# Optimization experiments

Hardware: AMD Instinct MI355X
Metric: run time of the kernel (lower is better)

## Reference

```python
import jax, jax.numpy as jnp
import numpy as np

B, N, DEG = 128, 512, 16          # graphs, nodes/graph, avg degree
NB = B * N                        # 65536 nodes
E = NB * DEG                      # 1048576 edges
K1, K2, K3 = 410, 205, 103        # ceil(0.8*512), ceil(0.5*410), ceil(0.5*205)
H, C = 4, 32                      # GAT heads, head dim
F_IN, ED = 128, 7


def _glorot(key, shape, fan_in):
    return jax.random.normal(key, shape, dtype=jnp.float32) / np.float32(np.sqrt(fan_in))


def setup_inputs() -> dict:
    key = jax.random.key(0)
    ks = jax.random.split(key, 24)
    x = jax.random.normal(ks[0], (NB, F_IN), dtype=jnp.float32)
    # random intra-graph edges, then offset per graph
    src = jax.random.randint(ks[1], (E,), 0, N)
    dst = jax.random.randint(ks[2], (E,), 0, N)
    off = jnp.repeat(jnp.arange(B) * N, N * DEG)
    edge_index = jnp.stack([src + off, dst + off]).astype(jnp.int32)
    edge_attr = jax.random.normal(ks[3], (E, ED), dtype=jnp.float32)
    p = {
        'c1_wl': _glorot(ks[4], (F_IN, F_IN), F_IN), 'c1_bl': jnp.zeros((F_IN,), jnp.float32), 'c1_wr': _glorot(ks[5], (F_IN, F_IN), F_IN),
        'p1_w': _glorot(ks[6], (F_IN,), F_IN),
        'c2_wl': _glorot(ks[7], (F_IN, F_IN), F_IN), 'c2_bl': jnp.zeros((F_IN,), jnp.float32), 'c2_wr': _glorot(ks[8], (F_IN, F_IN), F_IN),
        'p2_wrel': _glorot(ks[9], (F_IN, 1), F_IN), 'p2_brel': jnp.zeros((1,), jnp.float32), 'p2_wroot': _glorot(ks[10], (F_IN, 1), F_IN),
        'g_w': _glorot(ks[11], (F_IN, H * C), F_IN), 'g_as': _glorot(ks[12], (H, C), C), 'g_ad': _glorot(ks[13], (H, C), C),
        'g_we': _glorot(ks[14], (ED, H * C), ED), 'g_ae': _glorot(ks[15], (H, C), C), 'g_b': jnp.zeros((H * C,), jnp.float32),
        'p3_wrel': _glorot(ks[16], (F_IN, 1), F_IN), 'p3_brel': jnp.zeros((1,), jnp.float32), 'p3_wroot': _glorot(ks[17], (F_IN, 1), F_IN),
        'l1_w': _glorot(ks[18], (F_IN, F_IN), F_IN), 'l1_b': jnp.zeros((F_IN,), jnp.float32),
        'l2_w': _glorot(ks[19], (F_IN, 64), F_IN), 'l2_b': jnp.zeros((64,), jnp.float32),
        'l3_w': _glorot(ks[20], (64, 1), 64), 'l3_b': jnp.zeros((1,), jnp.float32),
    }
    return {'x': x, 'edge_index': edge_index, 'edge_attr': edge_attr, **p}


def _sage(x, src, dst, emf, wl, bl, wr):
    # SAGEConv: mean-aggregate neighbors (masked edges), lin_l(agg)+lin_r(x)
    agg = jax.ops.segment_sum(x[src] * emf[:, None], dst, num_segments=NB)
    cnt = jax.ops.segment_sum(emf, dst, num_segments=NB)
    mean = agg / jnp.maximum(cnt, 1.0)[:, None]
    return mean @ wl + bl + x @ wr


def _graphconv(x, src, dst, emf, wrel, brel, wroot):
    # GraphConv (SAGPooling score GNN): add-aggregation
    agg = jax.ops.segment_sum(x[src] * emf[:, None], dst, num_segments=NB)
    return (agg @ wrel + brel + x @ wroot).reshape(-1)


def _pool(x, score, nmask, K):
    # per-graph static top-k (equal-size graphs) == PyG topk + filter
    masked = jnp.where(nmask, score, -jnp.inf).reshape(B, N)
    idx = jax.lax.top_k(masked, K)[1]
    nm = jnp.zeros((B, N), dtype=bool).at[jnp.arange(B)[:, None], idx].set(True).reshape(-1)
    x = jnp.where(nm[:, None], x * score[:, None], 0.0)
    return x, nm


def _gap(x, K):
    # global mean pool; dropped nodes are exactly zero, K live nodes per graph
    return x.reshape(B, N, F_IN).sum(axis=1) / K


def _gat(x, src, dst, emf, nmask, edge_attr, w, a_s, a_d, w_e, a_e, b):
    xs = (x @ w).reshape(NB, H, C)
    al_s = (xs * a_s).sum(-1)                                   # [NB,H]
    al_d = (xs * a_d).sum(-1)
    al_e = ((edge_attr @ w_e).reshape(E, H, C) * a_e).sum(-1)    # [E,H]
    alpha = jax.nn.leaky_relu(al_s[src] + al_d[dst] + al_e, 0.2)
    alpha = jnp.where(emf[:, None] > 0, alpha, -jnp.inf)
    # PyG add_self_loops=True with fill_value='mean' for edge_attr
    ea_mean = (edge_attr * emf[:, None]).sum(0) / jnp.maximum(emf.sum(), 1.0)
    al_se = ((ea_mean @ w_e).reshape(H, C) * a_e).sum(-1)        # [H]
    alpha_self = jax.nn.leaky_relu(al_s + al_d + al_se[None, :], 0.2)
    alpha_self = jnp.where(nmask[:, None], alpha_self, -jnp.inf)
    m = jnp.maximum(jax.ops.segment_max(alpha, dst, num_segments=NB), alpha_self)
    m = jnp.where(jnp.isfinite(m), m, 0.0)
    ex = jnp.exp(alpha - m[dst]) * emf[:, None]
    ex_s = jnp.where(nmask[:, None], jnp.exp(alpha_self - m), 0.0)
    den = jnp.maximum(jax.ops.segment_sum(ex, dst, num_segments=NB) + ex_s, 1e-16)
    num = jax.ops.segment_sum(ex[:, :, None] * xs[src], dst, num_segments=NB) + ex_s[:, :, None] * xs
    return (num / den[:, :, None]).reshape(NB, H * C) + b


def _forward(x, edge_index, edge_attr, c1_wl, c1_bl, c1_wr, p1_w, c2_wl, c2_bl, c2_wr,
             p2_wrel, p2_brel, p2_wroot, g_w, g_as, g_ad, g_we, g_ae, g_b,
             p3_wrel, p3_brel, p3_wroot, l1_w, l1_b, l2_w, l2_b, l3_w, l3_b):
    src, dst = edge_index[0], edge_index[1]
    nmask = jnp.ones((NB,), dtype=bool)
    emf = jnp.ones((E,), jnp.float32)

    # block 1: SAGEConv -> TopKPooling(0.8) -> gap
    x = jax.nn.relu(_sage(x, src, dst, emf, c1_wl, c1_bl, c1_wr))
    s1 = jnp.tanh((x @ p1_w) / jnp.linalg.norm(p1_w))
    x, nmask = _pool(x, s1, nmask, K1)
    emf = emf * nmask[src] * nmask[dst]
    x1 = _gap(x, K1)

    # block 2: SAGEConv -> SAGPooling(0.5) -> gap
    x = jax.nn.relu(_sage(x, src, dst, emf, c2_wl, c2_bl, c2_wr))
    s2 = jnp.tanh(_graphconv(x, src, dst, emf, p2_wrel, p2_brel, p2_wroot))
    x, nmask = _pool(x, s2, nmask, K2)
    emf = emf * nmask[src] * nmask[dst]
    x2 = _gap(x, K2)

    # block 3: GATConv(128->32x4, edge_dim=7) -> SAGPooling(0.5) -> gap
    x = jax.nn.relu(_gat(x, src, dst, emf, nmask, edge_attr, g_w, g_as, g_ad, g_we, g_ae, g_b))
    s3 = jnp.tanh(_graphconv(x, src, dst, emf, p3_wrel, p3_brel, p3_wroot))
    x, nmask = _pool(x, s3, nmask, K3)
    x3 = _gap(x, K3)

    h = x1 + x2 + x3
    h = jax.nn.relu(h @ l1_w + l1_b)
    h = jax.nn.relu(h @ l2_w + l2_b)   # dropout identity in eval
    return jax.nn.sigmoid(h @ l3_w + l3_b)[:, 0]


def reference(x, edge_index, edge_attr, c1_wl, c1_bl, c1_wr, p1_w, c2_wl, c2_bl, c2_wr,
              p2_wrel, p2_brel, p2_wroot, g_w, g_as, g_ad, g_we, g_ae, g_b,
              p3_wrel, p3_brel, p3_wroot, l1_w, l1_b, l2_w, l2_b, l3_w, l3_b):
    return _forward(x, edge_index, edge_attr, c1_wl, c1_bl, c1_wr, p1_w, c2_wl, c2_bl, c2_wr,
                    p2_wrel, p2_brel, p2_wroot, g_w, g_as, g_ad, g_we, g_ae, g_b,
                    p3_wrel, p3_brel, p3_wroot, l1_w, l1_b, l2_w, l2_b, l3_w, l3_b)
```

## Files before the change

kernel.cpp:

```cpp
#include <hip/hip_runtime.h>
#include <math.h>

#define NBV 65536
#define EV  1048576
#define BV  128
#define K1V 410
#define K2V 205
#define K3V 103
#define NL1 (BV*K1V)
#define NL2 (BV*K2V)
#define NEG_BIG (-1.0e38f)

__device__ __forceinline__ float lrelu(float x){ return x > 0.f ? x : 0.2f*x; }

__global__ void k_init1(float* nmask, int* dcnt, int* fill, float* out, float sval){
  int i = blockIdx.x*blockDim.x + threadIdx.x;
  if (i < 128) out[i] = sval;
  if (i < NBV) nmask[i] = 1.f;
  if (i < NBV+1){ dcnt[i] = 0; fill[i] = 0; }
}

__global__ void k_hist(const int* dst, int* dcnt){
  int e = blockIdx.x*blockDim.x + threadIdx.x;
  if (e < EV) atomicAdd(&dcnt[dst[e]], 1);
}

__global__ void k_scan1(const int* dcnt, int* rp, int* bsum){
  __shared__ int sc[256];
  int t = threadIdx.x, i = blockIdx.x*256 + t;
  int v = dcnt[i];
  sc[t] = v; __syncthreads();
  for (int o = 1; o < 256; o <<= 1){
    int x = (t >= o) ? sc[t-o] : 0;
    __syncthreads();
    sc[t] += x;
    __syncthreads();
  }
  rp[i] = sc[t];
  if (t == 255) bsum[blockIdx.x] = sc[t];
}

__global__ void k_scan2(int* bsum){
  __shared__ int sc[256];
  int t = threadIdx.x;
  int v = bsum[t];
  sc[t] = v; __syncthreads();
  for (int o = 1; o < 256; o <<= 1){
    int x = (t >= o) ? sc[t-o] : 0;
    __syncthreads();
    sc[t] += x;
    __syncthreads();
  }
  bsum[t] = sc[t] - v;
}

__global__ void k_scan3(int* rp, const int* dcnt, const int* bsum){
  int t = threadIdx.x, i = blockIdx.x*256 + t;
  rp[i] = rp[i] - dcnt[i] + bsum[blockIdx.x];
  if (i == 0) rp[NBV] = EV;
}

__global__ void k_scatter(const int* src, const int* dst, const int* rp, int* fill,
                          int* csr_src, int* csr_eid){
  int e = blockIdx.x*blockDim.x + threadIdx.x;
  if (e < EV){
    int d = dst[e];
    int pos = atomicAdd(&fill[d], 1);
    int slot = rp[d] + pos;
    csr_src[slot] = src[e];
    csr_eid[slot] = e;
  }
}

__global__ void k_ve_inv(const float* g_we, const float* g_ae, const float* p1w, float* sml){
  __shared__ float sc[128];
  int t = threadIdx.x;
  if (t < 28){
    int ed = t >> 2, h = t & 3;
    float a = 0.f;
    for (int c = 0; c < 32; c++) a += g_we[ed*128 + h*32 + c] * g_ae[h*32 + c];
    sml[20 + t] = a;
  }
  float v = p1w[t];
  sc[t] = v*v; __syncthreads();
  for (int o = 64; o > 0; o >>= 1){ if (t < o) sc[t] += sc[t+o]; __syncthreads(); }
  if (t == 0) sml[0] = 1.f / sqrtf(sc[0]);
}

__global__ void k_ale(const float* ea, const float* ve, float* ALE){
  int e = blockIdx.x*blockDim.x + threadIdx.x;
  if (e < EV){
    float a0=0.f,a1=0.f,a2=0.f,a3=0.f;
    for (int ed = 0; ed < 7; ed++){
      float x = ea[e*7 + ed];
      a0 += x*ve[ed*4+0]; a1 += x*ve[ed*4+1]; a2 += x*ve[ed*4+2]; a3 += x*ve[ed*4+3];
    }
    float4 o; o.x=a0; o.y=a1; o.z=a2; o.w=a3;
    *(float4*)&ALE[(size_t)e*4] = o;
  }
}

__global__ void __launch_bounds__(256) k_sage_agg(const float* X, const float* nmask,
    const int* rp, const int* csr_src, float* AGG, int masked,
    const int* nidx, int kper){
  int g = blockIdx.x & 127;
  int blk = blockIdx.x >> 7;
  int r = blk*8 + (threadIdx.x >> 5);
  int i;
  if (nidx){ if (r >= kper) return; i = nidx[g*kper + r]; }
  else i = g*512 + r;
  int c4 = threadIdx.x & 31;
  float ax=0.f,ay=0.f,az=0.f,aw=0.f,cnt=0.f;
  if (!masked || nmask[i] > 0.f){
    int r0 = rp[i], r1 = rp[i+1];
    int s = r0;
    for (; s + 4 <= r1; s += 4){
      int sn0 = csr_src[s+0], sn1 = csr_src[s+1], sn2 = csr_src[s+2], sn3 = csr_src[s+3];
      float nm0 = masked ? nmask[sn0] : 1.f;
      float nm1 = masked ? nmask[sn1] : 1.f;
      float nm2 = masked ? nmask[sn2] : 1.f;
      float nm3 = masked ? nmask[sn3] : 1.f;
      if (nm0 > 0.f){ float4 v = *(const float4*)&X[((size_t)sn0 << 7) + (c4 << 2)];
                      ax += v.x; ay += v.y; az += v.z; aw += v.w; cnt += 1.f; }
      if (nm1 > 0.f){ float4 v = *(const float4*)&X[((size_t)sn1 << 7) + (c4 << 2)];
                      ax += v.x; ay += v.y; az += v.z; aw += v.w; cnt += 1.f; }
      if (nm2 > 0.f){ float4 v = *(const float4*)&X[((size_t)sn2 << 7) + (c4 << 2)];
                      ax += v.x; ay += v.y; az += v.z; aw += v.w; cnt += 1.f; }
      if (nm3 > 0.f){ float4 v = *(const float4*)&X[((size_t)sn3 << 7) + (c4 << 2)];
                      ax += v.x; ay += v.y; az += v.z; aw += v.w; cnt += 1.f; }
    }
    for (; s < r1; s++){
      int sn = csr_src[s];
      float nm = masked ? nmask[sn] : 1.f;
      if (nm > 0.f){
        const float4 v = *(const float4*)&X[((size_t)sn << 7) + (c4 << 2)];
        ax += v.x; ay += v.y; az += v.z; aw += v.w; cnt += 1.f;
      }
    }
  }
  float inv = 1.f / fmaxf(cnt, 1.f);
  float4 o; o.x = ax*inv; o.y = ay*inv; o.z = az*inv; o.w = aw*inv;
  *(float4*)&AGG[((size_t)i << 7) + (c4 << 2)] = o;
}

__global__ void __launch_bounds__(512) k_gemm(const float* A1, const float* A2,
    const float* W1, const float* W2, const float* bias,
    float* OUT, int has2, int relu, int hasb,
    const int* ridx, int sc_mode,
    const float* sw1, const float* sw2, const float* sinv,
    float* so1, float* so2){
  __shared__ float ws[128][128];
  __shared__ float as[16][136];
  int t = threadIdx.x;
  int n0 = blockIdx.x * 128;
  int rowg = t >> 5;
  int colg = t & 31;
  int rb = rowg * 8;
  int jb = colg * 4;
  int an = t >> 2;
  int ak = (t & 3) << 2;
  int arow = ridx ? ridx[n0 + an] : (n0 + an);
  float acc[8][4];
  for (int r = 0; r < 8; r++)
    for (int j = 0; j < 4; j++) acc[r][j] = 0.f;
  int nmat = has2 ? 2 : 1;
  for (int m = 0; m < nmat; m++){
    const float* A = (m == 0) ? A1 : A2;
    const float* W = (m == 0) ? W1 : W2;
    __syncthreads();
    for (int ii = 0; ii < 8; ii++){
      int idx4 = t + 512*ii;
      int kk = idx4 >> 5;
      int jj = (idx4 & 31) << 2;
      *(float4*)&ws[kk][jj] = *(const float4*)&W[kk*128 + jj];
    }
    float4 rA = *(const float4*)&A[((size_t)arow << 7) + ak];
    for (int c = 0; c < 8; c++){
      if (c > 0) __syncthreads();
      as[ak+0][an] = rA.x;
      as[ak+1][an] = rA.y;
      as[ak+2][an] = rA.z;
      as[ak+3][an] = rA.w;
      __syncthreads();
      if (c+1 < 8)
        rA = *(const float4*)&A[((size_t)arow << 7) + (c+1)*16 + ak];
      int kb = c*16;
      for (int kk = 0; kk < 16; kk++){
        float4 wv = *(const float4*)&ws[kb+kk][jb];
        float4 aL = *(const float4*)&as[kk][rb];
        float4 aH = *(const float4*)&as[kk][rb+4];
        float a0=aL.x,a1=aL.y,a2=aL.z,a3=aL.w,a4=aH.x,a5=aH.y,a6=aH.z,a7=aH.w;
        acc[0][0]+=a0*wv.x; acc[0][1]+=a0*wv.y; acc[0][2]+=a0*wv.z; acc[0][3]+=a0*wv.w;
        acc[1][0]+=a1*wv.x; acc[1][1]+=a1*wv.y; acc[1][2]+=a1*wv.z; acc[1][3]+=a1*wv.w;
        acc[2][0]+=a2*wv.x; acc[2][1]+=a2*wv.y; acc[2][2]+=a2*wv.z; acc[2][3]+=a2*wv.w;
        acc[3][0]+=a3*wv.x; acc[3][1]+=a3*wv.y; acc[3][2]+=a3*wv.z; acc[3][3]+=a3*wv.w;
        acc[4][0]+=a4*wv.x; acc[4][1]+=a4*wv.y; acc[4][2]+=a4*wv.z; acc[4][3]+=a4*wv.w;
        acc[5][0]+=a5*wv.x; acc[5][1]+=a5*wv.y; acc[5][2]+=a5*wv.z; acc[5][3]+=a5*wv.w;
        acc[6][0]+=a6*wv.x; acc[6][1]+=a6*wv.y; acc[6][2]+=a6*wv.z; acc[6][3]+=a6*wv.w;
        acc[7][0]+=a7*wv.x; acc[7][1]+=a7*wv.y; acc[7][2]+=a7*wv.z; acc[7][3]+=a7*wv.w;
      }
    }
  }
  float bj0=0.f,bj1=0.f,bj2=0.f,bj3=0.f;
  if (hasb){
    bj0 = bias[jb+0]; bj1 = bias[jb+1]; bj2 = bias[jb+2]; bj3 = bias[jb+3];
  }
  int orow[8];
  for (int r = 0; r < 8; r++) orow[r] = ridx ? ridx[n0+rb+r] : (n0+rb+r);
  float w1x=0.f,w1y=0.f,w1z=0.f,w1w=0.f, w2x=0.f,w2y=0.f,w2z=0.f,w2w=0.f;
  if (sc_mode){
    float4 t1 = *(const float4*)&sw1[jb];
    w1x=t1.x; w1y=t1.y; w1z=t1.z; w1w=t1.w;
    if (sc_mode >= 2){
      float4 t2 = *(const float4*)&sw2[jb];
      w2x=t2.x; w2y=t2.y; w2z=t2.z; w2w=t2.w;
    }
  }
  float pd1[8], pd2[8];
  for (int r = 0; r < 8; r++){
    float4 o;
    o.x = acc[r][0]+bj0; o.y = acc[r][1]+bj1; o.z = acc[r][2]+bj2; o.w = acc[r][3]+bj3;
    if (relu){
      o.x = fmaxf(o.x,0.f); o.y = fmaxf(o.y,0.f); o.z = fmaxf(o.z,0.f); o.w = fmaxf(o.w,0.f);
    }
    if (sc_mode){
      pd1[r] = o.x*w1x + o.y*w1y + o.z*w1z + o.w*w1w;
      if (sc_mode >= 2) pd2[r] = o.x*w2x + o.y*w2y + o.z*w2z + o.w*w2w;
    }
    *(float4*)&OUT[((size_t)orow[r] << 7) + jb] = o;
  }
  if (sc_mode == 1){
    float inv = sinv[0];
    for (int r = 0; r < 8; r++){
      float a = pd1[r];
      for (int o = 16; o > 0; o >>= 1) a += __shfl_down(a, o, 32);
      if (colg == 0) so1[orow[r]] = tanhf(a * inv);
    }
  } else if (sc_mode == 2){
    for (int r = 0; r < 8; r++){
      float a = pd1[r];
      float b = pd2[r];
      for (int o = 16; o > 0; o >>= 1){
        a += __shfl_down(a, o, 32);
        b += __shfl_down(b, o, 32);
      }
      if (colg == 0){ so1[orow[r]] = a; so2[orow[r]] = b; }
    }
  } else if (sc_mode == 3){
    int base = colg & ~7;
    for (int r = 0; r < 8; r++){
      float s1 = 0.f, s2 = 0.f;
      for (int c4 = 0; c4 < 8; c4++){
        s1 += __shfl(pd1[r], base + c4, 32);
        s2 += __shfl(pd2[r], base + c4, 32);
      }
      if ((colg & 7) == 0){
        int h = colg >> 3;
        so1[orow[r]*4 + h] = s1;
        so2[orow[r]*4 + h] = s2;
      }
    }
  }
}

__global__ void k_gconv(const float* q, const float* r, const float* nmask,
    const int* rp, const int* csr_src, const float* brel, float* s,
    const int* nidx, int ntot){
  int gid = blockIdx.x*blockDim.x + threadIdx.x;
  int i;
  if (nidx){ if (gid >= ntot) return; i = nidx[gid]; }
  else { if (gid >= NBV) return; i = gid; }
  float acc = 0.f;
  if (nmask[i] > 0.f){
    int r0 = rp[i], r1 = rp[i+1];
    int t2 = r0;
    for (; t2 + 4 <= r1; t2 += 4){
      int sn0 = csr_src[t2+0], sn1 = csr_src[t2+1], sn2 = csr_src[t2+2], sn3 = csr_src[t2+3];
      float nm0 = nmask[sn0], nm1 = nmask[sn1], nm2 = nmask[sn2], nm3 = nmask[sn3];
      if (nm0 > 0.f) acc += q[sn0];
      if (nm1 > 0.f) acc += q[sn1];
      if (nm2 > 0.f) acc += q[sn2];
      if (nm3 > 0.f) acc += q[sn3];
    }
    for (; t2 < r1; t2++){
      int sn = csr_src[t2];
      if (nmask[sn] > 0.f) acc += q[sn];
    }
  }
  s[i] = tanhf(acc + brel[0] + r[i]);
}

__global__ void __launch_bounds__(512) k_poolscale(const float* s, float* nmask,
    float* X, float* gap, int K, int* cidx, float invK){
  __shared__ float sc[512];
  __shared__ float lsel[512];
  __shared__ float prt[8][128];
  int b = blockIdx.x, t = threadIdx.x;
  int i = b*512 + t;
  float nm = nmask[i];
  float sv = s[i];
  float ms = (nm > 0.f) ? sv : NEG_BIG;
  sc[t] = ms;
  __syncthreads();
  int rank = 0;
  for (int j = 0; j < 512; j++){
    float o = sc[j];
    rank += ((o > ms) || (o == ms && j < t)) ? 1 : 0;
  }
  bool selb = rank < K;
  nmask[i] = selb ? 1.f : 0.f;
  if (cidx && selb) cidx[b*K + rank] = i;
  __syncthreads();
  sc[t] = selb ? 1.f : 0.f;
  lsel[t] = selb ? sv : 0.f;
  __syncthreads();
  int c = t & 127, g = t >> 7;
  for (int qq = 0; qq < 2; qq++){
    int q = g*2 + qq;
    float acc = 0.f;
    for (int n = q*64; n < q*64 + 64; n++){
      if (sc[n] > 0.f){
        size_t idx = (((size_t)(b*512 + n)) << 7) + c;
        float v = X[idx] * lsel[n];
        X[idx] = v;
        acc += v;
      }
    }
    prt[q][c] = acc;
  }
  __syncthreads();
  if (t < 128){
    float ss = 0.f;
    for (int q = 0; q < 8; q++) ss += prt[q][t];
    gap[b*128 + t] = ss * invK;
  }
}

__global__ void __launch_bounds__(256) k_ea_part(const float* ea, const int* srcA, const int* dstA,
    const float* nmask, float* part){
  float p[8] = {0.f,0.f,0.f,0.f,0.f,0.f,0.f,0.f};
  for (int e = blockIdx.x*256 + threadIdx.x; e < EV; e += 256*256){
    if (nmask[srcA[e]] > 0.f && nmask[dstA[e]] > 0.f){
      for (int d = 0; d < 7; d++) p[d] += ea[e*7 + d];
      p[7] += 1.f;
    }
  }
  __shared__ float red[256];
  for (int comp = 0; comp < 8; comp++){
    red[threadIdx.x] = p[comp]; __syncthreads();
    for (int o = 128; o > 0; o >>= 1){ if (threadIdx.x < o) red[threadIdx.x] += red[threadIdx.x + o]; __syncthreads(); }
    if (threadIdx.x == 0) part[blockIdx.x*8 + comp] = red[0];
    __syncthreads();
  }
}

__global__ void k_ea_fin(const float* part, const float* ve, float* alse){
  __shared__ float es[8];
  int h = threadIdx.x;
  if (h < 8){
    float s = 0.f;
    for (int b = 0; b < 256; b++) s += part[b*8 + h];
    es[h] = s;
  }
  __syncthreads();
  if (h == 0){
    float cnt = fmaxf(es[7], 1.f);
    for (int hh = 0; hh < 4; hh++){
      float s = 0.f;
      for (int ed = 0; ed < 7; ed++) s += (es[ed]/cnt) * ve[ed*4 + hh];
      alse[hh] = s;
    }
  }
}

__global__ void __launch_bounds__(256) k_gat(const float* xs, const float* alS, const float* alD,
    const float* ALE, const float* nmask, const int* rp, const int* csr_src,
    const int* csr_eid, const float* alse, const float* g_b,
    const float* wrel, const float* wroot, const int* nidx, int kper,
    float* qv, float* rv, float* OUT){
  int g = blockIdx.x & 127;
  int blk = blockIdx.x >> 7;
  int r = blk*8 + (threadIdx.x >> 5);
  int i;
  if (nidx){ if (r >= kper) return; i = nidx[g*kper + r]; }
  else i = g*512 + r;
  int lane = threadIdx.x & 31;
  int h = lane >> 3;
  int ch = h*8 + (lane & 7);
  float nmi = nmask[i];
  const float4* xs4 = (const float4*)xs;
  float m = 0.f, den = 0.f;
  float4 acc; acc.x=0.f; acc.y=0.f; acc.z=0.f; acc.w=0.f;
  if (nmi > 0.f){
    float ald_i = alD[i*4 + h];
    m = lrelu(alS[i*4 + h] + ald_i + alse[h]);
    den = 1.f;
    acc = xs4[(size_t)i*32 + ch];
    int r0 = rp[i], r1 = rp[i+1];
    int s = r0;
    for (; s + 4 <= r1; s += 4){
      int sn0 = csr_src[s+0], sn1 = csr_src[s+1], sn2 = csr_src[s+2], sn3 = csr_src[s+3];
      float nm0 = nmask[sn0], nm1 = nmask[sn1], nm2 = nmask[sn2], nm3 = nmask[sn3];
      if (nm0 > 0.f){
        float a = lrelu(alS[sn0*4 + h] + ald_i + ALE[(size_t)csr_eid[s+0]*4 + h]);
        float4 v = xs4[(size_t)sn0*32 + ch];
        float mn = fmaxf(m, a); float pm = expf(m - mn); float pa = expf(a - mn);
        den = den*pm + pa;
        acc.x = acc.x*pm + pa*v.x; acc.y = acc.y*pm + pa*v.y;
        acc.z = acc.z*pm + pa*v.z; acc.w = acc.w*pm + pa*v.w;
        m = mn;
      }
      if (nm1 > 0.f){
        float a = lrelu(alS[sn1*4 + h] + ald_i + ALE[(size_t)csr_eid[s+1]*4 + h]);
        float4 v = xs4[(size_t)sn1*32 + ch];
        float mn = fmaxf(m, a); float pm = expf(m - mn); float pa = expf(a - mn);
        den = den*pm + pa;
        acc.x = acc.x*pm + pa*v.x; acc.y = acc.y*pm + pa*v.y;
        acc.z = acc.z*pm + pa*v.z; acc.w = acc.w*pm + pa*v.w;
        m = mn;
      }
      if (nm2 > 0.f){
        float a = lrelu(alS[sn2*4 + h] + ald_i + ALE[(size_t)csr_eid[s+2]*4 + h]);
        float4 v = xs4[(size_t)sn2*32 + ch];
        float mn = fmaxf(m, a); float pm = expf(m - mn); float pa = expf(a - mn);
        den = den*pm + pa;
        acc.x = acc.x*pm + pa*v.x; acc.y = acc.y*pm + pa*v.y;
        acc.z = acc.z*pm + pa*v.z; acc.w = acc.w*pm + pa*v.w;
        m = mn;
      }
      if (nm3 > 0.f){
        float a = lrelu(alS[sn3*4 + h] + ald_i + ALE[(size_t)csr_eid[s+3]*4 + h]);
        float4 v = xs4[(size_t)sn3*32 + ch];
        float mn = fmaxf(m, a); float pm = expf(m - mn); float pa = expf(a - mn);
        den = den*pm + pa;
        acc.x = acc.x*pm + pa*v.x; acc.y = acc.y*pm + pa*v.y;
        acc.z = acc.z*pm + pa*v.z; acc.w = acc.w*pm + pa*v.w;
        m = mn;
      }
    }
    for (; s < r1; s++){
      int sn = csr_src[s];
      if (nmask[sn] > 0.f){
        float a = lrelu(alS[sn*4 + h] + ald_i + ALE[(size_t)csr_eid[s]*4 + h]);
        float4 v = xs4[(size_t)sn*32 + ch];
        float mn = fmaxf(m, a); float pm = expf(m - mn); float pa = expf(a - mn);
        den = den*pm + pa;
        acc.x = acc.x*pm + pa*v.x; acc.y = acc.y*pm + pa*v.y;
        acc.z = acc.z*pm + pa*v.z; acc.w = acc.w*pm + pa*v.w;
        m = mn;
      }
    }
  }
  den = fmaxf(den, 1e-16f);
  float rd = 1.f/den;
  int cb = ch << 2;
  float4 o;
  o.x = fmaxf(acc.x*rd + g_b[cb+0], 0.f);
  o.y = fmaxf(acc.y*rd + g_b[cb+1], 0.f);
  o.z = fmaxf(acc.z*rd + g_b[cb+2], 0.f);
  o.w = fmaxf(acc.w*rd + g_b[cb+3], 0.f);
  *(float4*)&OUT[((size_t)i << 7) + cb] = o;
  float4 wa = *(const float4*)&wrel[cb];
  float4 wb = *(const float4*)&wroot[cb];
  float aq = o.x*wa.x + o.y*wa.y + o.z*wa.z + o.w*wa.w;
  float ar = o.x*wb.x + o.y*wb.y + o.z*wb.z + o.w*wb.w;
  for (int off = 16; off > 0; off >>= 1){
    aq += __shfl_down(aq, off, 32);
    ar += __shfl_down(ar, off, 32);
  }
  if (lane == 0){ qv[i] = aq; rv[i] = ar; }
}

__global__ void __launch_bounds__(128) k_mlp(const float* x1g, const float* x2g, const float* x3g,
    const float* l1w, const float* l1b, const float* l2w, const float* l2b,
    const float* l3w, const float* l3b, float* out){
  __shared__ float hh[128];
  __shared__ float h2[128];
  __shared__ float h3[64];
  int b = blockIdx.x, t = threadIdx.x;
  hh[t] = x1g[b*128 + t] + x2g[b*128 + t] + x3g[b*128 + t];
  __syncthreads();
  float a = l1b[t];
  for (int k = 0; k < 128; k++) a += hh[k] * l1w[k*128 + t];
  h2[t] = fmaxf(a, 0.f);
  __syncthreads();
  if (t < 64){
    float a2 = l2b[t];
    for (int k = 0; k < 128; k++) a2 += h2[k] * l2w[k*64 + t];
    h3[t] = fmaxf(a2, 0.f);
  }
  __syncthreads();
  if (t == 0){
    float z = l3b[0];
    for (int k = 0; k < 64; k++) z += h3[k] * l3w[k];
    out[b] = 1.f/(1.f + expf(-z));
  }
}

extern "C" void kernel_launch(void* const* d_in, const int* in_sizes, int n_in,
                              void* d_out, int out_size, void* d_ws, size_t ws_size,
                              hipStream_t stream){
  const float* x       = (const float*)d_in[0];
  const int*   ei      = (const int*)d_in[1];
  const float* ea      = (const float*)d_in[2];
  const float* c1_wl   = (const float*)d_in[3];
  const float* c1_bl   = (const float*)d_in[4];
  const float* c1_wr   = (const float*)d_in[5];
  const float* p1_w    = (const float*)d_in[6];
  const float* c2_wl   = (const float*)d_in[7];
  const float* c2_bl   = (const float*)d_in[8];
  const float* c2_wr   = (const float*)d_in[9];
  const float* p2_wrel = (const float*)d_in[10];
  const float* p2_brel = (const float*)d_in[11];
  const float* p2_wroot= (const float*)d_in[12];
  const float* g_w     = (const float*)d_in[13];
  const float* g_as    = (const float*)d_in[14];
  const float* g_ad    = (const float*)d_in[15];
  const float* g_we    = (const float*)d_in[16];
  const float* g_ae    = (const float*)d_in[17];
  const float* g_b     = (const float*)d_in[18];
  const float* p3_wrel = (const float*)d_in[19];
  const float* p3_brel = (const float*)d_in[20];
  const float* p3_wroot= (const float*)d_in[21];
  const float* l1_w    = (const float*)d_in[22];
  const float* l1_b    = (const float*)d_in[23];
  const float* l2_w    = (const float*)d_in[24];
  const float* l2_b    = (const float*)d_in[25];
  const float* l3_w    = (const float*)d_in[26];
  const float* l3_b    = (const float*)d_in[27];
  float* out = (float*)d_out;
  (void)in_sizes; (void)n_in; (void)out_size;

  char* w = (char*)d_ws;
  size_t off = 0;
  float* AGG  = (float*)(w + off); off += (size_t)NBV*128*4;
  float* F1   = (float*)(w + off); off += (size_t)NBV*128*4;
  float* F2   = (float*)(w + off); off += (size_t)NBV*128*4;
  float* ALE  = (float*)(w + off); off += (size_t)EV*4*4;
  float* sA   = (float*)(w + off); off += (size_t)NBV*4;
  float* qv   = (float*)(w + off); off += (size_t)NBV*4;
  float* rv   = (float*)(w + off); off += (size_t)NBV*4;
  float* nmask= (float*)(w + off); off += (size_t)NBV*4;
  float* alS  = (float*)(w + off); off += (size_t)NBV*4*4;
  float* alD  = (float*)(w + off); off += (size_t)NBV*4*4;
  float* x1g  = (float*)(w + off); off += (size_t)BV*128*4;
  float* x2g  = (float*)(w + off); off += (size_t)BV*128*4;
  float* x3g  = (float*)(w + off); off += (size_t)BV*128*4;
  float* sml  = (float*)(w + off); off += 64*4;
  float* eprt = (float*)(w + off); off += 2048*4;
  int* csr_src = (int*)(w + off); off += (size_t)EV*4;
  int* csr_eid = (int*)(w + off); off += (size_t)EV*4;
  int* rp      = (int*)(w + off); off += (size_t)(NBV+64)*4;
  int* dcnt    = (int*)(w + off); off += (size_t)(NBV+64)*4;
  int* fill    = (int*)(w + off); off += (size_t)(NBV+64)*4;
  int* cidx1   = (int*)(w + off); off += (size_t)NBV*4;
  int* cidx2   = (int*)(w + off); off += (size_t)NBV*4;
  int* bsum    = (int*)(w + off); off += 1024;
  size_t needed = off;

  float sentinel = (ws_size >= needed) ? 0.125f : 0.875f;

  const int* srcA = ei;
  const int* dstA = ei + EV;

  k_init1<<<(NBV+256)/256, 256, 0, stream>>>(nmask, dcnt, fill, out, sentinel);
  k_hist<<<EV/256, 256, 0, stream>>>(dstA, dcnt);
  k_scan1<<<256, 256, 0, stream>>>(dcnt, rp, bsum);
  k_scan2<<<1, 256, 0, stream>>>(bsum);
  k_scan3<<<256, 256, 0, stream>>>(rp, dcnt, bsum);
  k_scatter<<<EV/256, 256, 0, stream>>>(srcA, dstA, rp, fill, csr_src, csr_eid);
  k_ve_inv<<<1, 128, 0, stream>>>(g_we, g_ae, p1_w, sml);
  k_ale<<<EV/256, 256, 0, stream>>>(ea, sml+20, ALE);

  k_sage_agg<<<(NBV*32)/256, 256, 0, stream>>>(x, nmask, rp, csr_src, AGG, 0,
                                               (const int*)nullptr, 512);
  k_gemm<<<NBV/128, 512, 0, stream>>>(AGG, x, c1_wl, c1_wr, c1_bl, F1, 1, 1, 1,
                                      (const int*)nullptr, 1, p1_w, (const float*)nullptr, sml, sA, (float*)nullptr);
  k_poolscale<<<BV, 512, 0, stream>>>(sA, nmask, F1, x1g, K1V, cidx1, 1.f/(float)K1V);

  k_sage_agg<<<BV*52, 256, 0, stream>>>(F1, nmask, rp, csr_src, AGG, 1, cidx1, K1V);
  k_gemm<<<NL1/128, 512, 0, stream>>>(AGG, F1, c2_wl, c2_wr, c2_bl, F2, 1, 1, 1,
                                      cidx1, 2, p2_wrel, p2_wroot, (const float*)nullptr, qv, rv);
  k_gconv<<<NL1/256, 256, 0, stream>>>(qv, rv, nmask, rp, csr_src, p2_brel, sA, cidx1, NL1);
  k_poolscale<<<BV, 512, 0, stream>>>(sA, nmask, F2, x2g, K2V, cidx2, 1.f/(float)K2V);

  k_gemm<<<NL2/128, 512, 0, stream>>>(F2, F2, g_w, g_w, g_b, AGG, 0, 0, 0,
                                      cidx2, 3, g_as, g_ad,
                                      (const float*)nullptr, alS, alD);
  k_ea_part<<<256, 256, 0, stream>>>(ea, srcA, dstA, nmask, eprt);
  k_ea_fin<<<1, 64, 0, stream>>>(eprt, sml+20, sml+16);
  k_gat<<<BV*26, 256, 0, stream>>>(AGG, alS, alD, ALE, nmask, rp, csr_src, csr_eid,
                                   sml+16, g_b, p3_wrel, p3_wroot, cidx2, K2V, qv, rv, F1);
  k_gconv<<<(NL2+255)/256, 256, 0, stream>>>(qv, rv, nmask, rp, csr_src, p3_brel, sA, cidx2, NL2);
  k_poolscale<<<BV, 512, 0, stream>>>(sA, nmask, F1, x3g, K3V, (int*)nullptr, 1.f/(float)K3V);

  k_mlp<<<BV, 128, 0, stream>>>(x1g, x2g, x3g, l1_w, l1_b, l2_w, l2_b, l3_w, l3_b, out);
}
```

Measured before the change: 685.5 us.

## Fuse GraphConv scoring into pooling kernel and merge CSR scatter with edge-attention precompute

The CSR scatter and the per-edge attention projection (ALE) become one edge-parallel kernel, removing a launch and a second pass over edge indices. The GraphConv score kernel is folded into the pooling kernel: each graph's block stages q and the node mask in shared memory, then each thread sums its in-graph neighbours locally before ranking. This drops two more launches and the global round trip of the score array. In exchange, score computation now runs only across 128 blocks of 512 threads, with less parallelism than the separate kernel had, and the pooling kernel uses more shared memory.

```diff
diff --git a/kernel.cpp b/kernel.cpp
--- a/kernel.cpp
+++ b/kernel.cpp
@@ -60,18 +60,6 @@
   if (i == 0) rp[NBV] = EV;
 }
 
-__global__ void k_scatter(const int* src, const int* dst, const int* rp, int* fill,
-                          int* csr_src, int* csr_eid){
-  int e = blockIdx.x*blockDim.x + threadIdx.x;
-  if (e < EV){
-    int d = dst[e];
-    int pos = atomicAdd(&fill[d], 1);
-    int slot = rp[d] + pos;
-    csr_src[slot] = src[e];
-    csr_eid[slot] = e;
-  }
-}
-
 __global__ void k_ve_inv(const float* g_we, const float* g_ae, const float* p1w, float* sml){
   __shared__ float sc[128];
   int t = threadIdx.x;
@@ -87,13 +75,20 @@
   if (t == 0) sml[0] = 1.f / sqrtf(sc[0]);
 }
 
-__global__ void k_ale(const float* ea, const float* ve, float* ALE){
+__global__ void k_scatter_ale(const int* src, const int* dst, const int* rp, int* fill,
+                              int* csr_src, int* csr_eid,
+                              const float* ea, const float* ve, float* ALE){
   int e = blockIdx.x*blockDim.x + threadIdx.x;
   if (e < EV){
+    int d = dst[e];
+    int pos = atomicAdd(&fill[d], 1);
+    int slot = rp[d] + pos;
+    csr_src[slot] = src[e];
+    csr_eid[slot] = e;
     float a0=0.f,a1=0.f,a2=0.f,a3=0.f;
     for (int ed = 0; ed < 7; ed++){
-      float x = ea[e*7 + ed];
-      a0 += x*ve[ed*4+0]; a1 += x*ve[ed*4+1]; a2 += x*ve[ed*4+2]; a3 += x*ve[ed*4+3];
+      float x2 = ea[e*7 + ed];
+      a0 += x2*ve[ed*4+0]; a1 += x2*ve[ed*4+1]; a2 += x2*ve[ed*4+2]; a3 += x2*ve[ed*4+3];
     }
     float4 o; o.x=a0; o.y=a1; o.z=a2; o.w=a3;
     *(float4*)&ALE[(size_t)e*4] = o;
@@ -263,42 +258,36 @@
   }
 }
 
-__global__ void k_gconv(const float* q, const float* r, const float* nmask,
-    const int* rp, const int* csr_src, const float* brel, float* s,
-    const int* nidx, int ntot){
-  int gid = blockIdx.x*blockDim.x + threadIdx.x;
-  int i;
-  if (nidx){ if (gid >= ntot) return; i = nidx[gid]; }
-  else { if (gid >= NBV) return; i = gid; }
-  float acc = 0.f;
-  if (nmask[i] > 0.f){
-    int r0 = rp[i], r1 = rp[i+1];
-    int t2 = r0;
-    for (; t2 + 4 <= r1; t2 += 4){
-      int sn0 = csr_src[t2+0], sn1 = csr_src[t2+1], sn2 = csr_src[t2+2], sn3 = csr_src[t2+3];
-      float nm0 = nmask[sn0], nm1 = nmask[sn1], nm2 = nmask[sn2], nm3 = nmask[sn3];
-      if (nm0 > 0.f) acc += q[sn0];
-      if (nm1 > 0.f) acc += q[sn1];
-      if (nm2 > 0.f) acc += q[sn2];
-      if (nm3 > 0.f) acc += q[sn3];
-    }
-    for (; t2 < r1; t2++){
-      int sn = csr_src[t2];
-      if (nmask[sn] > 0.f) acc += q[sn];
-    }
-  }
-  s[i] = tanhf(acc + brel[0] + r[i]);
-}
-
-__global__ void __launch_bounds__(512) k_poolscale(const float* s, float* nmask,
-    float* X, float* gap, int K, int* cidx, float invK){
+__global__ void __launch_bounds__(512) k_poolscale(const float* sIn,
+    const float* qv, const float* rv, const float* brel,
+    const int* rp, const int* csr_src,
+    float* nmask, float* X, float* gap, int K, int* cidx, float invK, int mode){
+  __shared__ float qls[512];
+  __shared__ float nml[512];
   __shared__ float sc[512];
   __shared__ float lsel[512];
   __shared__ float prt[8][128];
   int b = blockIdx.x, t = threadIdx.x;
   int i = b*512 + t;
   float nm = nmask[i];
-  float sv = s[i];
+  float sv = 0.f;
+  if (mode){
+    qls[t] = qv[i];
+    nml[t] = nm;
+    __syncthreads();
+    if (nm > 0.f){
+      float acc = 0.f;
+      int r0 = rp[i], r1 = rp[i+1];
+      int base = b*512;
+      for (int s = r0; s < r1; s++){
+        int ln = csr_src[s] - base;
+        if (nml[ln] > 0.f) acc += qls[ln];
+      }
+      sv = tanhf(acc + brel[0] + rv[i]);
+    }
+  } else {
+    sv = sIn[i];
+  }
   float ms = (nm > 0.f) ? sv : NEG_BIG;
   sc[t] = ms;
   __syncthreads();
@@ -568,21 +557,23 @@
   k_scan1<<<256, 256, 0, stream>>>(dcnt, rp, bsum);
   k_scan2<<<1, 256, 0, stream>>>(bsum);
   k_scan3<<<256, 256, 0, stream>>>(rp, dcnt, bsum);
-  k_scatter<<<EV/256, 256, 0, stream>>>(srcA, dstA, rp, fill, csr_src, csr_eid);
   k_ve_inv<<<1, 128, 0, stream>>>(g_we, g_ae, p1_w, sml);
-  k_ale<<<EV/256, 256, 0, stream>>>(ea, sml+20, ALE);
+  k_scatter_ale<<<EV/256, 256, 0, stream>>>(srcA, dstA, rp, fill, csr_src, csr_eid,
+                                            ea, sml+20, ALE);
 
   k_sage_agg<<<(NBV*32)/256, 256, 0, stream>>>(x, nmask, rp, csr_src, AGG, 0,
                                                (const int*)nullptr, 512);
   k_gemm<<<NBV/128, 512, 0, stream>>>(AGG, x, c1_wl, c1_wr, c1_bl, F1, 1, 1, 1,
                                       (const int*)nullptr, 1, p1_w, (const float*)nullptr, sml, sA, (float*)nullptr);
-  k_poolscale<<<BV, 512, 0, stream>>>(sA, nmask, F1, x1g, K1V, cidx1, 1.f/(float)K1V);
+  k_poolscale<<<BV, 512, 0, stream>>>(sA, (const float*)nullptr, (const float*)nullptr,
+                                      (const float*)nullptr, (const int*)nullptr, (const int*)nullptr,
+                                      nmask, F1, x1g, K1V, cidx1, 1.f/(float)K1V, 0);
 
   k_sage_agg<<<BV*52, 256, 0, stream>>>(F1, nmask, rp, csr_src, AGG, 1, cidx1, K1V);
   k_gemm<<<NL1/128, 512, 0, stream>>>(AGG, F1, c2_wl, c2_wr, c2_bl, F2, 1, 1, 1,
                                       cidx1, 2, p2_wrel, p2_wroot, (const float*)nullptr, qv, rv);
-  k_gconv<<<NL1/256, 256, 0, stream>>>(qv, rv, nmask, rp, csr_src, p2_brel, sA, cidx1, NL1);
-  k_poolscale<<<BV, 512, 0, stream>>>(sA, nmask, F2, x2g, K2V, cidx2, 1.f/(float)K2V);
+  k_poolscale<<<BV, 512, 0, stream>>>((const float*)nullptr, qv, rv, p2_brel, rp, csr_src,
+                                      nmask, F2, x2g, K2V, cidx2, 1.f/(float)K2V, 1);
 
   k_gemm<<<NL2/128, 512, 0, stream>>>(F2, F2, g_w, g_w, g_b, AGG, 0, 0, 0,
                                       cidx2, 3, g_as, g_ad,
@@ -591,8 +582,8 @@
   k_ea_fin<<<1, 64, 0, stream>>>(eprt, sml+20, sml+16);
   k_gat<<<BV*26, 256, 0, stream>>>(AGG, alS, alD, ALE, nmask, rp, csr_src, csr_eid,
                                    sml+16, g_b, p3_wrel, p3_wroot, cidx2, K2V, qv, rv, F1);
-  k_gconv<<<(NL2+255)/256, 256, 0, stream>>>(qv, rv, nmask, rp, csr_src, p3_brel, sA, cidx2, NL2);
-  k_poolscale<<<BV, 512, 0, stream>>>(sA, nmask, F1, x3g, K3V, (int*)nullptr, 1.f/(float)K3V);
+  k_poolscale<<<BV, 512, 0, stream>>>((const float*)nullptr, qv, rv, p3_brel, rp, csr_src,
+                                      nmask, F1, x3g, K3V, (int*)nullptr, 1.f/(float)K3V, 1);
 
   k_mlp<<<BV, 128, 0, stream>>>(x1g, x2g, x3g, l1_w, l1_b, l2_w, l2_b, l3_w, l3_b, out);
 }
```

Result: faster. 671.0 us (-2.1%).
